# Kernel optimization log

Measured on AMD Instinct MI355X. Metric: run time of the kernel, lower is better.

The kernel has to match this reference:

```python
import jax, jax.numpy as jnp
import numpy as np

P, G, N = 32, 256, 6890  # preds, gallery size, SMPL vertices per person


def _procrustes_v2v(pred, gt):
    """Similarity (Procrustes) align pred->gt, return mean per-vertex L2 error.
    pred, gt: (M, 3) point clouds (M = 2*N, both people jointly aligned)."""
    mu_p = pred.mean(axis=0)
    mu_g = gt.mean(axis=0)
    Xp = pred - mu_p
    Xg = gt - mu_g
    var_p = jnp.sum(Xp * Xp)
    K = Xp.T @ Xg                      # (3,3) cross-covariance
    U, s, Vh = jnp.linalg.svd(K)
    V = Vh.T
    d = jnp.sign(jnp.linalg.det(V @ U.T))  # reflection fix
    D = jnp.stack([jnp.ones_like(d), jnp.ones_like(d), d])
    R = (V * D[None, :]) @ U.T         # rotation, det(R)=+1
    scale = jnp.sum(s * D) / var_p
    aligned = scale * (Xp @ R.T) + mu_g
    return jnp.linalg.norm(aligned - gt, axis=-1).mean()


def setup_inputs() -> dict:
    key = jax.random.key(0)
    k1, k2 = jax.random.split(key)
    pred_vertices = jax.random.normal(k1, (P, 2, N, 3), dtype=jnp.float32)
    target = jax.random.normal(k2, (G, 2, N, 3), dtype=jnp.float32)
    return {"pred_vertices": pred_vertices, "target": target}


def reference(pred_vertices, target):
    # flatten the two-person meshes into a single joint point cloud per sample
    pred = pred_vertices.reshape(pred_vertices.shape[0], -1, 3)  # (P, 2N, 3)
    gt = target.reshape(target.shape[0], -1, 3)                  # (G, 2N, 3)
    # all-pairs procrustes v2v errors: (P, G)
    pair_err = jax.vmap(lambda p: jax.vmap(lambda g: _procrustes_v2v(p, g))(gt))(pred)
    mapping = jnp.argmin(pair_err, axis=1)   # best gt index per prediction
    min_error = jnp.min(pair_err, axis=1)    # its v2v error
    return mapping, min_error
```

## Files before the change

kernel.cpp:

```cpp
#include <hip/hip_runtime.h>
#include <math.h>

#define P_ 32
#define G_ 256
#define NV 6890
#define M_ (2 * NV)
#define QUADS (M_ / 4)
#define NPAIR (P_ * G_)
#define NB_CC 512

struct WS {
    float mu_p[P_][3];
    float var_p[P_];
    float mu_g[G_][3];
    float At[NPAIR][12];
    float Kmat[NPAIR][9];
    float pair_err[NPAIR];
};

__device__ inline double block_reduce(double v, double* smem) {
#pragma unroll
    for (int off = 32; off > 0; off >>= 1) v += __shfl_down(v, off, 64);
    int wid  = threadIdx.x >> 6;
    int lane = threadIdx.x & 63;
    __syncthreads();
    if (lane == 0) smem[wid] = v;
    __syncthreads();
    double r = 0.0;
    if (threadIdx.x == 0) {
        int nw = blockDim.x >> 6;
        for (int w = 0; w < nw; ++w) r += smem[w];
    }
    return r;
}

#define LOAD_QUAD(BASE, Q, X, Y, Z)                                     \
    {                                                                   \
        const float4* _p4 = (const float4*)((BASE) + 12 * (size_t)(Q)); \
        float4 _a = _p4[0], _c = _p4[1], _d = _p4[2];                   \
        X[0] = _a.x; X[1] = _a.w; X[2] = _c.z; X[3] = _d.y;             \
        Y[0] = _a.y; Y[1] = _c.x; Y[2] = _c.w; Y[3] = _d.z;             \
        Z[0] = _a.z; Z[1] = _c.y; Z[2] = _d.x; Z[3] = _d.w;             \
    }

__global__ __launch_bounds__(256, 2) void crosscov_r(const float* __restrict__ pred,
                                                     const float* __restrict__ gt,
                                                     WS* __restrict__ ws) {
    int bx = blockIdx.x;
    int t = threadIdx.x;

    if (bx >= NB_CC) {
        int b = bx - NB_CC;
        bool isP = (b < P_);
        const float* base = isP ? pred + (size_t)b * (M_ * 3)
                                : gt + (size_t)(b - P_) * (M_ * 3);
        double sx = 0, sy = 0, sz = 0, sq = 0;
        for (int q = t; q < QUADS; q += 256) {
            const float4* p4 = (const float4*)(base + 12 * (size_t)q);
            float4 a = p4[0], c = p4[1], d = p4[2];
            sx += (double)a.x + (double)a.w + (double)c.z + (double)d.y;
            sy += (double)a.y + (double)c.x + (double)c.w + (double)d.z;
            sz += (double)a.z + (double)c.y + (double)d.x + (double)d.w;
            if (isP) {
                sq += (double)a.x * a.x + (double)a.y * a.y + (double)a.z * a.z +
                      (double)a.w * a.w + (double)c.x * c.x + (double)c.y * c.y +
                      (double)c.z * c.z + (double)c.w * c.w + (double)d.x * d.x +
                      (double)d.y * d.y + (double)d.z * d.z + (double)d.w * d.w;
            }
        }
        __shared__ double smem[4];
        double rx = block_reduce(sx, smem);
        double ry = block_reduce(sy, smem);
        double rz = block_reduce(sz, smem);
        double rq = block_reduce(sq, smem);
        if (t == 0) {
            double mx = rx / M_, my = ry / M_, mz = rz / M_;
            if (isP) {
                ws->mu_p[b][0] = (float)mx;
                ws->mu_p[b][1] = (float)my;
                ws->mu_p[b][2] = (float)mz;
                ws->var_p[b] = (float)(rq - (mx * mx + my * my + mz * mz) * (double)M_);
            } else {
                ws->mu_g[b - P_][0] = (float)mx;
                ws->mu_g[b - P_][1] = (float)my;
                ws->mu_g[b - P_][2] = (float)mz;
            }
        }
        return;
    }

    int gbase = (bx & 63) * 4;
    int pbase = (bx >> 6) * 4;
    const float* pb[4];
    const float* gb[4];
#pragma unroll
    for (int j = 0; j < 4; ++j) {
        pb[j] = pred + (size_t)(pbase + j) * (M_ * 3);
        gb[j] = gt + (size_t)(gbase + j) * (M_ * 3);
    }

    float acc[16][9];
#pragma unroll
    for (int q = 0; q < 16; ++q)
#pragma unroll
        for (int j = 0; j < 9; ++j) acc[q][j] = 0.f;

    for (int q = t; q < QUADS; q += 256) {
        float px[4][4], py[4][4], pz[4][4];
#pragma unroll
        for (int j = 0; j < 4; ++j) LOAD_QUAD(pb[j], q, px[j], py[j], pz[j]);
#pragma unroll
        for (int gg = 0; gg < 4; ++gg) {
            float gx[4], gy[4], gz[4];
            LOAD_QUAD(gb[gg], q, gx, gy, gz);
#pragma unroll
            for (int pp = 0; pp < 4; ++pp) {
                float* a = acc[gg * 4 + pp];
#pragma unroll
                for (int k = 0; k < 4; ++k) {
                    a[0] = fmaf(px[pp][k], gx[k], a[0]);
                    a[1] = fmaf(px[pp][k], gy[k], a[1]);
                    a[2] = fmaf(px[pp][k], gz[k], a[2]);
                    a[3] = fmaf(py[pp][k], gx[k], a[3]);
                    a[4] = fmaf(py[pp][k], gy[k], a[4]);
                    a[5] = fmaf(py[pp][k], gz[k], a[5]);
                    a[6] = fmaf(pz[pp][k], gx[k], a[6]);
                    a[7] = fmaf(pz[pp][k], gy[k], a[7]);
                    a[8] = fmaf(pz[pp][k], gz[k], a[8]);
                }
            }
        }
    }

#pragma unroll
    for (int q = 0; q < 16; ++q)
#pragma unroll
        for (int j = 0; j < 9; ++j) {
            float v = acc[q][j];
            v += __shfl_xor(v, 1);  v += __shfl_xor(v, 2);
            v += __shfl_xor(v, 4);  v += __shfl_xor(v, 8);
            v += __shfl_xor(v, 16); v += __shfl_xor(v, 32);
            acc[q][j] = v;
        }
    __shared__ float part[4][144];
    int lane = t & 63, wave = t >> 6;
    if (lane == 0) {
#pragma unroll
        for (int q = 0; q < 16; ++q)
#pragma unroll
            for (int j = 0; j < 9; ++j) part[wave][q * 9 + j] = acc[q][j];
    }
    __syncthreads();
    if (t < 144) {
        float s = part[0][t] + part[1][t] + part[2][t] + part[3][t];
        int idx = t / 9, j = t % 9;
        int gg = idx >> 2, pp = idx & 3;
        ws->Kmat[(gbase + gg) * P_ + (pbase + pp)][j] = s;
    }
}

__global__ __launch_bounds__(64) void pair_svd(WS* ws) {
    int pair = blockIdx.x * blockDim.x + threadIdx.x;
    if (pair >= NPAIR) return;
    int p = pair & 31;
    int g = pair >> 5;

    double K[3][3];
#pragma unroll
    for (int a = 0; a < 3; ++a)
#pragma unroll
        for (int b = 0; b < 3; ++b) K[a][b] = (double)ws->Kmat[pair][3 * a + b];
    {
        double mp[3] = { ws->mu_p[p][0], ws->mu_p[p][1], ws->mu_p[p][2] };
        double mg[3] = { ws->mu_g[g][0], ws->mu_g[g][1], ws->mu_g[g][2] };
#pragma unroll
        for (int a = 0; a < 3; ++a)
#pragma unroll
            for (int b = 0; b < 3; ++b)
                K[a][b] -= (double)M_ * mp[a] * mg[b];
    }

    double S[3][3];
#pragma unroll
    for (int a = 0; a < 3; ++a)
#pragma unroll
        for (int b = 0; b < 3; ++b) {
            double acc = 0.0;
#pragma unroll
            for (int c = 0; c < 3; ++c) acc += K[c][a] * K[c][b];
            S[a][b] = acc;
        }

    double V[3][3] = { {1, 0, 0}, {0, 1, 0}, {0, 0, 1} };
    double tr = S[0][0] + S[1][1] + S[2][2];
    double tol = 1e-26 * tr * tr + 1e-300;
    const int PP[3] = {0, 0, 1};
    const int QQ[3] = {1, 2, 2};
    for (int sweep = 0; sweep < 8; ++sweep) {
        double off = S[0][1] * S[0][1] + S[0][2] * S[0][2] + S[1][2] * S[1][2];
        if (off <= tol) break;
        for (int r3 = 0; r3 < 3; ++r3) {
            int pq = PP[r3], qq = QQ[r3];
            double apq = S[pq][qq];
            if (apq == 0.0) continue;
            double theta = (S[qq][qq] - S[pq][pq]) / (2.0 * apq);
            double tt = copysign(1.0, theta) / (fabs(theta) + sqrt(theta * theta + 1.0));
            double c = 1.0 / sqrt(tt * tt + 1.0);
            double sj = tt * c;
            for (int r = 0; r < 3; ++r) {
                double srp = S[r][pq], srq = S[r][qq];
                S[r][pq] = c * srp - sj * srq;
                S[r][qq] = sj * srp + c * srq;
            }
            for (int cc = 0; cc < 3; ++cc) {
                double spr = S[pq][cc], sqr = S[qq][cc];
                S[pq][cc] = c * spr - sj * sqr;
                S[qq][cc] = sj * spr + c * sqr;
            }
            for (int r = 0; r < 3; ++r) {
                double vrp = V[r][pq], vrq = V[r][qq];
                V[r][pq] = c * vrp - sj * vrq;
                V[r][qq] = sj * vrp + c * vrq;
            }
        }
    }

    double lam[3] = { S[0][0], S[1][1], S[2][2] };
    int idx[3] = { 0, 1, 2 };
    if (lam[idx[0]] < lam[idx[1]]) { int tt = idx[0]; idx[0] = idx[1]; idx[1] = tt; }
    if (lam[idx[0]] < lam[idx[2]]) { int tt = idx[0]; idx[0] = idx[2]; idx[2] = tt; }
    if (lam[idx[1]] < lam[idx[2]]) { int tt = idx[1]; idx[1] = idx[2]; idx[2] = tt; }
    double Vs[3][3];
    double sv[3];
#pragma unroll
    for (int i = 0; i < 3; ++i) {
        double l = lam[idx[i]];
        sv[i] = sqrt(l > 0.0 ? l : 0.0);
        for (int r = 0; r < 3; ++r) Vs[r][i] = V[r][idx[i]];
    }

    double U[3][3];
#pragma unroll
    for (int i = 0; i < 3; ++i) {
        double kx = K[0][0] * Vs[0][i] + K[0][1] * Vs[1][i] + K[0][2] * Vs[2][i];
        double ky = K[1][0] * Vs[0][i] + K[1][1] * Vs[1][i] + K[1][2] * Vs[2][i];
        double kz = K[2][0] * Vs[0][i] + K[2][1] * Vs[1][i] + K[2][2] * Vs[2][i];
        double inv = (sv[i] > 1e-12 * sv[0] && sv[i] > 0.0) ? 1.0 / sv[i] : 0.0;
        U[0][i] = kx * inv; U[1][i] = ky * inv; U[2][i] = kz * inv;
    }
    if (sv[2] <= 1e-12 * sv[0] || sv[0] == 0.0) {
        U[0][2] = U[1][0] * U[2][1] - U[2][0] * U[1][1];
        U[1][2] = U[2][0] * U[0][1] - U[0][0] * U[2][1];
        U[2][2] = U[0][0] * U[1][1] - U[1][0] * U[0][1];
    }

    double detK = K[0][0] * (K[1][1] * K[2][2] - K[1][2] * K[2][1])
                - K[0][1] * (K[1][0] * K[2][2] - K[1][2] * K[2][0])
                + K[0][2] * (K[1][0] * K[2][1] - K[1][1] * K[2][0]);
    double d = (detK >= 0.0) ? 1.0 : -1.0;

    double varp = (double)ws->var_p[p];
    double scale = (sv[0] + sv[1] + d * sv[2]) / varp;

    float A[9];
#pragma unroll
    for (int a = 0; a < 3; ++a)
#pragma unroll
        for (int b = 0; b < 3; ++b) {
            double r = Vs[a][0] * U[b][0] + Vs[a][1] * U[b][1] + d * Vs[a][2] * U[b][2];
            A[3 * a + b] = (float)(scale * r);
        }
    double mp[3] = { ws->mu_p[p][0], ws->mu_p[p][1], ws->mu_p[p][2] };
    double mg[3] = { ws->mu_g[g][0], ws->mu_g[g][1], ws->mu_g[g][2] };
    float tvec[3];
#pragma unroll
    for (int a = 0; a < 3; ++a)
        tvec[a] = (float)(mg[a] - ((double)A[3 * a + 0] * mp[0] + (double)A[3 * a + 1] * mp[1] +
                                   (double)A[3 * a + 2] * mp[2]));

#pragma unroll
    for (int j = 0; j < 9; ++j) ws->At[pair][j] = A[j];
#pragma unroll
    for (int j = 0; j < 3; ++j) ws->At[pair][9 + j] = tvec[j];
}

__global__ __launch_bounds__(256, 3) void pair_error_r(const float* __restrict__ pred,
                                                       const float* __restrict__ gt,
                                                       WS* __restrict__ ws) {
    int bx = blockIdx.x;
    int gbase = (bx & 63) * 4;
    int pbase = (bx >> 6) * 2;
    int t = threadIdx.x;

    float A[8][12];
#pragma unroll
    for (int gg = 0; gg < 4; ++gg)
#pragma unroll
        for (int pp = 0; pp < 2; ++pp) {
            int pair = (gbase + gg) * P_ + (pbase + pp);
#pragma unroll
            for (int j = 0; j < 12; ++j) A[gg * 2 + pp][j] = ws->At[pair][j];
        }

    const float* pb0 = pred + (size_t)pbase * (M_ * 3);
    const float* pb1 = pred + (size_t)(pbase + 1) * (M_ * 3);
    const float* gb[4];
#pragma unroll
    for (int j = 0; j < 4; ++j) gb[j] = gt + (size_t)(gbase + j) * (M_ * 3);

    float acc[8];
#pragma unroll
    for (int q = 0; q < 8; ++q) acc[q] = 0.f;

    for (int q = t; q < QUADS; q += 256) {
        float px[2][4], py[2][4], pz[2][4];
        LOAD_QUAD(pb0, q, px[0], py[0], pz[0]);
        LOAD_QUAD(pb1, q, px[1], py[1], pz[1]);
#pragma unroll
        for (int gg = 0; gg < 4; ++gg) {
            float gx[4], gy[4], gz[4];
            LOAD_QUAD(gb[gg], q, gx, gy, gz);
#pragma unroll
            for (int pp = 0; pp < 2; ++pp) {
                const float* a = A[gg * 2 + pp];
                float s = 0.f;
#pragma unroll
                for (int k = 0; k < 4; ++k) {
                    float dx = fmaf(a[0], px[pp][k], fmaf(a[1], py[pp][k], fmaf(a[2], pz[pp][k], a[9])))  - gx[k];
                    float dy = fmaf(a[3], px[pp][k], fmaf(a[4], py[pp][k], fmaf(a[5], pz[pp][k], a[10]))) - gy[k];
                    float dz = fmaf(a[6], px[pp][k], fmaf(a[7], py[pp][k], fmaf(a[8], pz[pp][k], a[11]))) - gz[k];
                    s += __builtin_amdgcn_sqrtf(fmaf(dx, dx, fmaf(dy, dy, dz * dz)));
                }
                acc[gg * 2 + pp] += s;
            }
        }
    }

#pragma unroll
    for (int q = 0; q < 8; ++q) {
        float v = acc[q];
        v += __shfl_xor(v, 1);  v += __shfl_xor(v, 2);
        v += __shfl_xor(v, 4);  v += __shfl_xor(v, 8);
        v += __shfl_xor(v, 16); v += __shfl_xor(v, 32);
        acc[q] = v;
    }
    __shared__ float part[4][8];
    int lane = t & 63, wave = t >> 6;
    if (lane == 0) {
#pragma unroll
        for (int q = 0; q < 8; ++q) part[wave][q] = acc[q];
    }
    __syncthreads();
    if (t < 8) {
        float s = part[0][t] + part[1][t] + part[2][t] + part[3][t];
        int gg = t >> 1, pp = t & 1;
        ws->pair_err[(gbase + gg) * P_ + (pbase + pp)] = s / (float)M_;
    }
}

__global__ void argmin_out(const WS* __restrict__ ws, float* __restrict__ out) {
    __shared__ float be[8][32];
    __shared__ int   bg[8][32];
    int t = threadIdx.x;
    int p = t & 31, slice = t >> 5;
    float best = 3.4e38f;
    int bi = G_;
    for (int g = slice; g < G_; g += 8) {
        float e = ws->pair_err[g * P_ + p];
        if (e < best) { best = e; bi = g; }
    }
    be[slice][p] = best;
    bg[slice][p] = bi;
    __syncthreads();
    if (t < P_) {
        float b0 = be[0][t];
        int   i0 = bg[0][t];
        for (int s = 1; s < 8; ++s) {
            float e = be[s][t];
            int   i = bg[s][t];
            if (e < b0 || (e == b0 && i < i0)) { b0 = e; i0 = i; }
        }
        out[t] = (float)i0;
        out[P_ + t] = b0;
    }
}

extern "C" void kernel_launch(void* const* d_in, const int* in_sizes, int n_in,
                              void* d_out, int out_size, void* d_ws, size_t ws_size,
                              hipStream_t stream) {
    const float* pred = (const float*)d_in[0];
    const float* gt   = (const float*)d_in[1];
    float* out = (float*)d_out;
    WS* ws = (WS*)d_ws;

    crosscov_r<<<dim3(NB_CC + P_ + G_), dim3(256), 0, stream>>>(pred, gt, ws);
    pair_svd<<<dim3(NPAIR / 64), dim3(64), 0, stream>>>(ws);
    pair_error_r<<<dim3(16 * 64), dim3(256), 0, stream>>>(pred, gt, ws);
    argmin_out<<<dim3(1), dim3(256), 0, stream>>>(ws, out);
}
```

Baseline: 214.6 us.

## Split vertex reduction into chunks and shrink crosscov tile to raise parallelism

The cross-covariance and pair-error kernels now split the vertex range into two chunks, each handled by its own block. Each block writes partial sums, which the SVD and argmin kernels combine. The crosscov tile also shrinks from 4x4 to 2x4 pairs with higher occupancy bounds, which lowers register pressure and multiplies block count. In exchange, data reuse per loaded point drops (pred points are reused across fewer pairs), global traffic rises, and partial buffers add extra writes and reads.

```diff
diff --git a/kernel.cpp b/kernel.cpp
--- a/kernel.cpp
+++ b/kernel.cpp
@@ -7,15 +7,16 @@
 #define M_ (2 * NV)
 #define QUADS (M_ / 4)
 #define NPAIR (P_ * G_)
-#define NB_CC 512
+#define KC 2
+#define NB_CC (16 * 64 * KC)
 
 struct WS {
     float mu_p[P_][3];
     float var_p[P_];
     float mu_g[G_][3];
     float At[NPAIR][12];
-    float Kmat[NPAIR][9];
-    float pair_err[NPAIR];
+    float partK[KC][NPAIR][9];
+    float partE[KC][NPAIR];
 };
 
 __device__ inline double block_reduce(double v, double* smem) {
@@ -43,7 +44,7 @@
         Z[0] = _a.z; Z[1] = _c.y; Z[2] = _d.x; Z[3] = _d.w;             \
     }
 
-__global__ __launch_bounds__(256, 2) void crosscov_r(const float* __restrict__ pred,
+__global__ __launch_bounds__(256, 3) void crosscov_c(const float* __restrict__ pred,
                                                      const float* __restrict__ gt,
                                                      WS* __restrict__ ws) {
     int bx = blockIdx.x;
@@ -89,33 +90,35 @@
         return;
     }
 
-    int gbase = (bx & 63) * 4;
-    int pbase = (bx >> 6) * 4;
-    const float* pb[4];
+    int kc = bx >> 10;
+    int rem = bx & 1023;
+    int gbase = (rem & 63) * 4;
+    int pbase = (rem >> 6) * 2;
+    int qbeg = (QUADS * kc) / KC, qend = (QUADS * (kc + 1)) / KC;
+
+    const float* pb0 = pred + (size_t)pbase * (M_ * 3);
+    const float* pb1 = pred + (size_t)(pbase + 1) * (M_ * 3);
     const float* gb[4];
 #pragma unroll
-    for (int j = 0; j < 4; ++j) {
-        pb[j] = pred + (size_t)(pbase + j) * (M_ * 3);
-        gb[j] = gt + (size_t)(gbase + j) * (M_ * 3);
-    }
-
-    float acc[16][9];
-#pragma unroll
-    for (int q = 0; q < 16; ++q)
+    for (int j = 0; j < 4; ++j) gb[j] = gt + (size_t)(gbase + j) * (M_ * 3);
+
+    float acc[8][9];
+#pragma unroll
+    for (int q = 0; q < 8; ++q)
 #pragma unroll
         for (int j = 0; j < 9; ++j) acc[q][j] = 0.f;
 
-    for (int q = t; q < QUADS; q += 256) {
-        float px[4][4], py[4][4], pz[4][4];
-#pragma unroll
-        for (int j = 0; j < 4; ++j) LOAD_QUAD(pb[j], q, px[j], py[j], pz[j]);
+    for (int q = qbeg + t; q < qend; q += 256) {
+        float px[2][4], py[2][4], pz[2][4];
+        LOAD_QUAD(pb0, q, px[0], py[0], pz[0]);
+        LOAD_QUAD(pb1, q, px[1], py[1], pz[1]);
 #pragma unroll
         for (int gg = 0; gg < 4; ++gg) {
             float gx[4], gy[4], gz[4];
             LOAD_QUAD(gb[gg], q, gx, gy, gz);
 #pragma unroll
-            for (int pp = 0; pp < 4; ++pp) {
-                float* a = acc[gg * 4 + pp];
+            for (int pp = 0; pp < 2; ++pp) {
+                float* a = acc[gg * 2 + pp];
 #pragma unroll
                 for (int k = 0; k < 4; ++k) {
                     a[0] = fmaf(px[pp][k], gx[k], a[0]);
@@ -133,7 +136,7 @@
     }
 
 #pragma unroll
-    for (int q = 0; q < 16; ++q)
+    for (int q = 0; q < 8; ++q)
 #pragma unroll
         for (int j = 0; j < 9; ++j) {
             float v = acc[q][j];
@@ -142,20 +145,20 @@
             v += __shfl_xor(v, 16); v += __shfl_xor(v, 32);
             acc[q][j] = v;
         }
-    __shared__ float part[4][144];
+    __shared__ float part[4][72];
     int lane = t & 63, wave = t >> 6;
     if (lane == 0) {
 #pragma unroll
-        for (int q = 0; q < 16; ++q)
+        for (int q = 0; q < 8; ++q)
 #pragma unroll
             for (int j = 0; j < 9; ++j) part[wave][q * 9 + j] = acc[q][j];
     }
     __syncthreads();
-    if (t < 144) {
+    if (t < 72) {
         float s = part[0][t] + part[1][t] + part[2][t] + part[3][t];
         int idx = t / 9, j = t % 9;
-        int gg = idx >> 2, pp = idx & 3;
-        ws->Kmat[(gbase + gg) * P_ + (pbase + pp)][j] = s;
+        int gg = idx >> 1, pp = idx & 1;
+        ws->partK[kc][(gbase + gg) * P_ + (pbase + pp)][j] = s;
     }
 }
 
@@ -169,7 +172,12 @@
 #pragma unroll
     for (int a = 0; a < 3; ++a)
 #pragma unroll
-        for (int b = 0; b < 3; ++b) K[a][b] = (double)ws->Kmat[pair][3 * a + b];
+        for (int b = 0; b < 3; ++b) {
+            double s = 0.0;
+#pragma unroll
+            for (int kc = 0; kc < KC; ++kc) s += (double)ws->partK[kc][pair][3 * a + b];
+            K[a][b] = s;
+        }
     {
         double mp[3] = { ws->mu_p[p][0], ws->mu_p[p][1], ws->mu_p[p][2] };
         double mg[3] = { ws->mu_g[g][0], ws->mu_g[g][1], ws->mu_g[g][2] };
@@ -284,12 +292,15 @@
     for (int j = 0; j < 3; ++j) ws->At[pair][9 + j] = tvec[j];
 }
 
-__global__ __launch_bounds__(256, 3) void pair_error_r(const float* __restrict__ pred,
+__global__ __launch_bounds__(256, 3) void pair_error_c(const float* __restrict__ pred,
                                                        const float* __restrict__ gt,
                                                        WS* __restrict__ ws) {
     int bx = blockIdx.x;
-    int gbase = (bx & 63) * 4;
-    int pbase = (bx >> 6) * 2;
+    int kc = bx >> 10;
+    int rem = bx & 1023;
+    int gbase = (rem & 63) * 4;
+    int pbase = (rem >> 6) * 2;
+    int qbeg = (QUADS * kc) / KC, qend = (QUADS * (kc + 1)) / KC;
     int t = threadIdx.x;
 
     float A[8][12];
@@ -312,7 +323,7 @@
 #pragma unroll
     for (int q = 0; q < 8; ++q) acc[q] = 0.f;
 
-    for (int q = t; q < QUADS; q += 256) {
+    for (int q = qbeg + t; q < qend; q += 256) {
         float px[2][4], py[2][4], pz[2][4];
         LOAD_QUAD(pb0, q, px[0], py[0], pz[0]);
         LOAD_QUAD(pb1, q, px[1], py[1], pz[1]);
@@ -354,7 +365,7 @@
     if (t < 8) {
         float s = part[0][t] + part[1][t] + part[2][t] + part[3][t];
         int gg = t >> 1, pp = t & 1;
-        ws->pair_err[(gbase + gg) * P_ + (pbase + pp)] = s / (float)M_;
+        ws->partE[kc][(gbase + gg) * P_ + (pbase + pp)] = s;
     }
 }
 
@@ -366,7 +377,10 @@
     float best = 3.4e38f;
     int bi = G_;
     for (int g = slice; g < G_; g += 8) {
-        float e = ws->pair_err[g * P_ + p];
+        double s = 0.0;
+#pragma unroll
+        for (int kc = 0; kc < KC; ++kc) s += (double)ws->partE[kc][g * P_ + p];
+        float e = (float)(s / (double)M_);
         if (e < best) { best = e; bi = g; }
     }
     be[slice][p] = best;
@@ -393,8 +407,8 @@
     float* out = (float*)d_out;
     WS* ws = (WS*)d_ws;
 
-    crosscov_r<<<dim3(NB_CC + P_ + G_), dim3(256), 0, stream>>>(pred, gt, ws);
+    crosscov_c<<<dim3(NB_CC + P_ + G_), dim3(256), 0, stream>>>(pred, gt, ws);
     pair_svd<<<dim3(NPAIR / 64), dim3(64), 0, stream>>>(ws);
-    pair_error_r<<<dim3(16 * 64), dim3(256), 0, stream>>>(pred, gt, ws);
+    pair_error_c<<<dim3(16 * 64 * KC), dim3(256), 0, stream>>>(pred, gt, ws);
     argmin_out<<<dim3(1), dim3(256), 0, stream>>>(ws, out);
 }
```

Result: no change. 211.6 us (-1.4%).

## Fuse mean/variance and per-pair SVD into cross-covariance kernel

Applied to the files above, without the earlier changes.

Merges the separate mean/variance blocks and the pair_svd kernel into the cross-covariance kernel. Each block now handles a 2x4 pred/gallery tile instead of 4x4, accumulates the point sums and squared norms alongside K, and then runs the 3x3 SVD for its 8 pairs in the epilogue. This removes one kernel launch and the workspace round-trip for K and the means. In exchange, pred and gallery means are recomputed redundantly in many blocks, gallery data is reloaded twice as often, the sums are kept in float rather than double, and the serial double-precision SVD tail runs on only 8 threads per block.

```diff
diff --git a/kernel.cpp b/kernel.cpp
--- a/kernel.cpp
+++ b/kernel.cpp
@@ -7,32 +7,11 @@
 #define M_ (2 * NV)
 #define QUADS (M_ / 4)
 #define NPAIR (P_ * G_)
-#define NB_CC 512
 
 struct WS {
-    float mu_p[P_][3];
-    float var_p[P_];
-    float mu_g[G_][3];
     float At[NPAIR][12];
-    float Kmat[NPAIR][9];
     float pair_err[NPAIR];
 };
-
-__device__ inline double block_reduce(double v, double* smem) {
-#pragma unroll
-    for (int off = 32; off > 0; off >>= 1) v += __shfl_down(v, off, 64);
-    int wid  = threadIdx.x >> 6;
-    int lane = threadIdx.x & 63;
-    __syncthreads();
-    if (lane == 0) smem[wid] = v;
-    __syncthreads();
-    double r = 0.0;
-    if (threadIdx.x == 0) {
-        int nw = blockDim.x >> 6;
-        for (int w = 0; w < nw; ++w) r += smem[w];
-    }
-    return r;
-}
 
 #define LOAD_QUAD(BASE, Q, X, Y, Z)                                     \
     {                                                                   \
@@ -43,79 +22,71 @@
         Z[0] = _a.z; Z[1] = _c.y; Z[2] = _d.x; Z[3] = _d.w;             \
     }
 
-__global__ __launch_bounds__(256, 2) void crosscov_r(const float* __restrict__ pred,
-                                                     const float* __restrict__ gt,
-                                                     WS* __restrict__ ws) {
+#define BFLY(v)                                              \
+    {                                                        \
+        v += __shfl_xor(v, 1);  v += __shfl_xor(v, 2);       \
+        v += __shfl_xor(v, 4);  v += __shfl_xor(v, 8);       \
+        v += __shfl_xor(v, 16); v += __shfl_xor(v, 32);      \
+    }
+
+__global__ __launch_bounds__(256, 3) void crosscov_svd(const float* __restrict__ pred,
+                                                       const float* __restrict__ gt,
+                                                       WS* __restrict__ ws) {
     int bx = blockIdx.x;
     int t = threadIdx.x;
-
-    if (bx >= NB_CC) {
-        int b = bx - NB_CC;
-        bool isP = (b < P_);
-        const float* base = isP ? pred + (size_t)b * (M_ * 3)
-                                : gt + (size_t)(b - P_) * (M_ * 3);
-        double sx = 0, sy = 0, sz = 0, sq = 0;
-        for (int q = t; q < QUADS; q += 256) {
-            const float4* p4 = (const float4*)(base + 12 * (size_t)q);
-            float4 a = p4[0], c = p4[1], d = p4[2];
-            sx += (double)a.x + (double)a.w + (double)c.z + (double)d.y;
-            sy += (double)a.y + (double)c.x + (double)c.w + (double)d.z;
-            sz += (double)a.z + (double)c.y + (double)d.x + (double)d.w;
-            if (isP) {
-                sq += (double)a.x * a.x + (double)a.y * a.y + (double)a.z * a.z +
-                      (double)a.w * a.w + (double)c.x * c.x + (double)c.y * c.y +
-                      (double)c.z * c.z + (double)c.w * c.w + (double)d.x * d.x +
-                      (double)d.y * d.y + (double)d.z * d.z + (double)d.w * d.w;
-            }
-        }
-        __shared__ double smem[4];
-        double rx = block_reduce(sx, smem);
-        double ry = block_reduce(sy, smem);
-        double rz = block_reduce(sz, smem);
-        double rq = block_reduce(sq, smem);
-        if (t == 0) {
-            double mx = rx / M_, my = ry / M_, mz = rz / M_;
-            if (isP) {
-                ws->mu_p[b][0] = (float)mx;
-                ws->mu_p[b][1] = (float)my;
-                ws->mu_p[b][2] = (float)mz;
-                ws->var_p[b] = (float)(rq - (mx * mx + my * my + mz * mz) * (double)M_);
-            } else {
-                ws->mu_g[b - P_][0] = (float)mx;
-                ws->mu_g[b - P_][1] = (float)my;
-                ws->mu_g[b - P_][2] = (float)mz;
-            }
-        }
-        return;
-    }
-
     int gbase = (bx & 63) * 4;
-    int pbase = (bx >> 6) * 4;
-    const float* pb[4];
+    int pbase = (bx >> 6) * 2;
+
+    const float* pb0 = pred + (size_t)pbase * (M_ * 3);
+    const float* pb1 = pred + (size_t)(pbase + 1) * (M_ * 3);
     const float* gb[4];
 #pragma unroll
-    for (int j = 0; j < 4; ++j) {
-        pb[j] = pred + (size_t)(pbase + j) * (M_ * 3);
-        gb[j] = gt + (size_t)(gbase + j) * (M_ * 3);
-    }
-
-    float acc[16][9];
-#pragma unroll
-    for (int q = 0; q < 16; ++q)
+    for (int j = 0; j < 4; ++j) gb[j] = gt + (size_t)(gbase + j) * (M_ * 3);
+
+    float acc[8][9];
+    float ps[2][4];
+    float gs[4][3];
+#pragma unroll
+    for (int q = 0; q < 8; ++q)
 #pragma unroll
         for (int j = 0; j < 9; ++j) acc[q][j] = 0.f;
+#pragma unroll
+    for (int q = 0; q < 2; ++q)
+#pragma unroll
+        for (int j = 0; j < 4; ++j) ps[q][j] = 0.f;
+#pragma unroll
+    for (int q = 0; q < 4; ++q)
+#pragma unroll
+        for (int j = 0; j < 3; ++j) gs[q][j] = 0.f;
 
     for (int q = t; q < QUADS; q += 256) {
-        float px[4][4], py[4][4], pz[4][4];
-#pragma unroll
-        for (int j = 0; j < 4; ++j) LOAD_QUAD(pb[j], q, px[j], py[j], pz[j]);
+        float px[2][4], py[2][4], pz[2][4];
+        LOAD_QUAD(pb0, q, px[0], py[0], pz[0]);
+        LOAD_QUAD(pb1, q, px[1], py[1], pz[1]);
+#pragma unroll
+        for (int pp = 0; pp < 2; ++pp)
+#pragma unroll
+            for (int k = 0; k < 4; ++k) {
+                ps[pp][0] += px[pp][k];
+                ps[pp][1] += py[pp][k];
+                ps[pp][2] += pz[pp][k];
+                ps[pp][3] = fmaf(px[pp][k], px[pp][k],
+                            fmaf(py[pp][k], py[pp][k],
+                            fmaf(pz[pp][k], pz[pp][k], ps[pp][3])));
+            }
 #pragma unroll
         for (int gg = 0; gg < 4; ++gg) {
             float gx[4], gy[4], gz[4];
             LOAD_QUAD(gb[gg], q, gx, gy, gz);
 #pragma unroll
-            for (int pp = 0; pp < 4; ++pp) {
-                float* a = acc[gg * 4 + pp];
+            for (int k = 0; k < 4; ++k) {
+                gs[gg][0] += gx[k];
+                gs[gg][1] += gy[k];
+                gs[gg][2] += gz[k];
+            }
+#pragma unroll
+            for (int pp = 0; pp < 2; ++pp) {
+                float* a = acc[gg * 2 + pp];
 #pragma unroll
                 for (int k = 0; k < 4; ++k) {
                     a[0] = fmaf(px[pp][k], gx[k], a[0]);
@@ -133,155 +104,160 @@
     }
 
 #pragma unroll
-    for (int q = 0; q < 16; ++q)
-#pragma unroll
-        for (int j = 0; j < 9; ++j) {
-            float v = acc[q][j];
-            v += __shfl_xor(v, 1);  v += __shfl_xor(v, 2);
-            v += __shfl_xor(v, 4);  v += __shfl_xor(v, 8);
-            v += __shfl_xor(v, 16); v += __shfl_xor(v, 32);
-            acc[q][j] = v;
-        }
-    __shared__ float part[4][144];
+    for (int q = 0; q < 8; ++q)
+#pragma unroll
+        for (int j = 0; j < 9; ++j) BFLY(acc[q][j]);
+#pragma unroll
+    for (int q = 0; q < 2; ++q)
+#pragma unroll
+        for (int j = 0; j < 4; ++j) BFLY(ps[q][j]);
+#pragma unroll
+    for (int q = 0; q < 4; ++q)
+#pragma unroll
+        for (int j = 0; j < 3; ++j) BFLY(gs[q][j]);
+
+    __shared__ float red[4][92];
+    __shared__ float fin[92];
     int lane = t & 63, wave = t >> 6;
     if (lane == 0) {
 #pragma unroll
-        for (int q = 0; q < 16; ++q)
-#pragma unroll
-            for (int j = 0; j < 9; ++j) part[wave][q * 9 + j] = acc[q][j];
+        for (int q = 0; q < 8; ++q)
+#pragma unroll
+            for (int j = 0; j < 9; ++j) red[wave][q * 9 + j] = acc[q][j];
+#pragma unroll
+        for (int q = 0; q < 2; ++q)
+#pragma unroll
+            for (int j = 0; j < 4; ++j) red[wave][72 + q * 4 + j] = ps[q][j];
+#pragma unroll
+        for (int q = 0; q < 4; ++q)
+#pragma unroll
+            for (int j = 0; j < 3; ++j) red[wave][80 + q * 3 + j] = gs[q][j];
     }
     __syncthreads();
-    if (t < 144) {
-        float s = part[0][t] + part[1][t] + part[2][t] + part[3][t];
-        int idx = t / 9, j = t % 9;
-        int gg = idx >> 2, pp = idx & 3;
-        ws->Kmat[(gbase + gg) * P_ + (pbase + pp)][j] = s;
-    }
-}
-
-__global__ __launch_bounds__(64) void pair_svd(WS* ws) {
-    int pair = blockIdx.x * blockDim.x + threadIdx.x;
-    if (pair >= NPAIR) return;
-    int p = pair & 31;
-    int g = pair >> 5;
-
-    double K[3][3];
-#pragma unroll
-    for (int a = 0; a < 3; ++a)
-#pragma unroll
-        for (int b = 0; b < 3; ++b) K[a][b] = (double)ws->Kmat[pair][3 * a + b];
-    {
-        double mp[3] = { ws->mu_p[p][0], ws->mu_p[p][1], ws->mu_p[p][2] };
-        double mg[3] = { ws->mu_g[g][0], ws->mu_g[g][1], ws->mu_g[g][2] };
+    if (t < 92) fin[t] = red[0][t] + red[1][t] + red[2][t] + red[3][t];
+    __syncthreads();
+
+    if (t < 8) {
+        int gg = t >> 1, pp = t & 1;
+        double K[3][3];
+#pragma unroll
+        for (int a = 0; a < 3; ++a)
+#pragma unroll
+            for (int b = 0; b < 3; ++b) K[a][b] = (double)fin[t * 9 + 3 * a + b];
+
+        double mp[3] = { fin[72 + pp * 4 + 0] / (double)M_,
+                         fin[72 + pp * 4 + 1] / (double)M_,
+                         fin[72 + pp * 4 + 2] / (double)M_ };
+        double varp = (double)fin[72 + pp * 4 + 3] -
+                      (mp[0] * mp[0] + mp[1] * mp[1] + mp[2] * mp[2]) * (double)M_;
+        double mg[3] = { fin[80 + gg * 3 + 0] / (double)M_,
+                         fin[80 + gg * 3 + 1] / (double)M_,
+                         fin[80 + gg * 3 + 2] / (double)M_ };
 #pragma unroll
         for (int a = 0; a < 3; ++a)
 #pragma unroll
             for (int b = 0; b < 3; ++b)
                 K[a][b] -= (double)M_ * mp[a] * mg[b];
-    }
-
-    double S[3][3];
-#pragma unroll
-    for (int a = 0; a < 3; ++a)
-#pragma unroll
-        for (int b = 0; b < 3; ++b) {
-            double acc = 0.0;
-#pragma unroll
-            for (int c = 0; c < 3; ++c) acc += K[c][a] * K[c][b];
-            S[a][b] = acc;
-        }
-
-    double V[3][3] = { {1, 0, 0}, {0, 1, 0}, {0, 0, 1} };
-    double tr = S[0][0] + S[1][1] + S[2][2];
-    double tol = 1e-26 * tr * tr + 1e-300;
-    const int PP[3] = {0, 0, 1};
-    const int QQ[3] = {1, 2, 2};
-    for (int sweep = 0; sweep < 8; ++sweep) {
-        double off = S[0][1] * S[0][1] + S[0][2] * S[0][2] + S[1][2] * S[1][2];
-        if (off <= tol) break;
-        for (int r3 = 0; r3 < 3; ++r3) {
-            int pq = PP[r3], qq = QQ[r3];
-            double apq = S[pq][qq];
-            if (apq == 0.0) continue;
-            double theta = (S[qq][qq] - S[pq][pq]) / (2.0 * apq);
-            double tt = copysign(1.0, theta) / (fabs(theta) + sqrt(theta * theta + 1.0));
-            double c = 1.0 / sqrt(tt * tt + 1.0);
-            double sj = tt * c;
-            for (int r = 0; r < 3; ++r) {
-                double srp = S[r][pq], srq = S[r][qq];
-                S[r][pq] = c * srp - sj * srq;
-                S[r][qq] = sj * srp + c * srq;
-            }
-            for (int cc = 0; cc < 3; ++cc) {
-                double spr = S[pq][cc], sqr = S[qq][cc];
-                S[pq][cc] = c * spr - sj * sqr;
-                S[qq][cc] = sj * spr + c * sqr;
-            }
-            for (int r = 0; r < 3; ++r) {
-                double vrp = V[r][pq], vrq = V[r][qq];
-                V[r][pq] = c * vrp - sj * vrq;
-                V[r][qq] = sj * vrp + c * vrq;
-            }
-        }
-    }
-
-    double lam[3] = { S[0][0], S[1][1], S[2][2] };
-    int idx[3] = { 0, 1, 2 };
-    if (lam[idx[0]] < lam[idx[1]]) { int tt = idx[0]; idx[0] = idx[1]; idx[1] = tt; }
-    if (lam[idx[0]] < lam[idx[2]]) { int tt = idx[0]; idx[0] = idx[2]; idx[2] = tt; }
-    if (lam[idx[1]] < lam[idx[2]]) { int tt = idx[1]; idx[1] = idx[2]; idx[2] = tt; }
-    double Vs[3][3];
-    double sv[3];
-#pragma unroll
-    for (int i = 0; i < 3; ++i) {
-        double l = lam[idx[i]];
-        sv[i] = sqrt(l > 0.0 ? l : 0.0);
-        for (int r = 0; r < 3; ++r) Vs[r][i] = V[r][idx[i]];
-    }
-
-    double U[3][3];
-#pragma unroll
-    for (int i = 0; i < 3; ++i) {
-        double kx = K[0][0] * Vs[0][i] + K[0][1] * Vs[1][i] + K[0][2] * Vs[2][i];
-        double ky = K[1][0] * Vs[0][i] + K[1][1] * Vs[1][i] + K[1][2] * Vs[2][i];
-        double kz = K[2][0] * Vs[0][i] + K[2][1] * Vs[1][i] + K[2][2] * Vs[2][i];
-        double inv = (sv[i] > 1e-12 * sv[0] && sv[i] > 0.0) ? 1.0 / sv[i] : 0.0;
-        U[0][i] = kx * inv; U[1][i] = ky * inv; U[2][i] = kz * inv;
-    }
-    if (sv[2] <= 1e-12 * sv[0] || sv[0] == 0.0) {
-        U[0][2] = U[1][0] * U[2][1] - U[2][0] * U[1][1];
-        U[1][2] = U[2][0] * U[0][1] - U[0][0] * U[2][1];
-        U[2][2] = U[0][0] * U[1][1] - U[1][0] * U[0][1];
-    }
-
-    double detK = K[0][0] * (K[1][1] * K[2][2] - K[1][2] * K[2][1])
-                - K[0][1] * (K[1][0] * K[2][2] - K[1][2] * K[2][0])
-                + K[0][2] * (K[1][0] * K[2][1] - K[1][1] * K[2][0]);
-    double d = (detK >= 0.0) ? 1.0 : -1.0;
-
-    double varp = (double)ws->var_p[p];
-    double scale = (sv[0] + sv[1] + d * sv[2]) / varp;
-
-    float A[9];
-#pragma unroll
-    for (int a = 0; a < 3; ++a)
-#pragma unroll
-        for (int b = 0; b < 3; ++b) {
-            double r = Vs[a][0] * U[b][0] + Vs[a][1] * U[b][1] + d * Vs[a][2] * U[b][2];
-            A[3 * a + b] = (float)(scale * r);
-        }
-    double mp[3] = { ws->mu_p[p][0], ws->mu_p[p][1], ws->mu_p[p][2] };
-    double mg[3] = { ws->mu_g[g][0], ws->mu_g[g][1], ws->mu_g[g][2] };
-    float tvec[3];
-#pragma unroll
-    for (int a = 0; a < 3; ++a)
-        tvec[a] = (float)(mg[a] - ((double)A[3 * a + 0] * mp[0] + (double)A[3 * a + 1] * mp[1] +
-                                   (double)A[3 * a + 2] * mp[2]));
-
-#pragma unroll
-    for (int j = 0; j < 9; ++j) ws->At[pair][j] = A[j];
-#pragma unroll
-    for (int j = 0; j < 3; ++j) ws->At[pair][9 + j] = tvec[j];
+
+        double S[3][3];
+#pragma unroll
+        for (int a = 0; a < 3; ++a)
+#pragma unroll
+            for (int b = 0; b < 3; ++b) {
+                double s = 0.0;
+#pragma unroll
+                for (int c = 0; c < 3; ++c) s += K[c][a] * K[c][b];
+                S[a][b] = s;
+            }
+
+        double V[3][3] = { {1, 0, 0}, {0, 1, 0}, {0, 0, 1} };
+        double tr = S[0][0] + S[1][1] + S[2][2];
+        double tol = 1e-26 * tr * tr + 1e-300;
+        const int PPi[3] = {0, 0, 1};
+        const int QQi[3] = {1, 2, 2};
+        for (int sweep = 0; sweep < 8; ++sweep) {
+            double off = S[0][1] * S[0][1] + S[0][2] * S[0][2] + S[1][2] * S[1][2];
+            if (off <= tol) break;
+            for (int r3 = 0; r3 < 3; ++r3) {
+                int pq = PPi[r3], qq = QQi[r3];
+                double apq = S[pq][qq];
+                if (apq == 0.0) continue;
+                double theta = (S[qq][qq] - S[pq][pq]) / (2.0 * apq);
+                double tt = copysign(1.0, theta) / (fabs(theta) + sqrt(theta * theta + 1.0));
+                double c = 1.0 / sqrt(tt * tt + 1.0);
+                double sj = tt * c;
+                for (int r = 0; r < 3; ++r) {
+                    double srp = S[r][pq], srq = S[r][qq];
+                    S[r][pq] = c * srp - sj * srq;
+                    S[r][qq] = sj * srp + c * srq;
+                }
+                for (int cc = 0; cc < 3; ++cc) {
+                    double spr = S[pq][cc], sqr = S[qq][cc];
+                    S[pq][cc] = c * spr - sj * sqr;
+                    S[qq][cc] = sj * spr + c * sqr;
+                }
+                for (int r = 0; r < 3; ++r) {
+                    double vrp = V[r][pq], vrq = V[r][qq];
+                    V[r][pq] = c * vrp - sj * vrq;
+                    V[r][qq] = sj * vrp + c * vrq;
+                }
+            }
+        }
+
+        double lam[3] = { S[0][0], S[1][1], S[2][2] };
+        int idx[3] = { 0, 1, 2 };
+        if (lam[idx[0]] < lam[idx[1]]) { int w = idx[0]; idx[0] = idx[1]; idx[1] = w; }
+        if (lam[idx[0]] < lam[idx[2]]) { int w = idx[0]; idx[0] = idx[2]; idx[2] = w; }
+        if (lam[idx[1]] < lam[idx[2]]) { int w = idx[1]; idx[1] = idx[2]; idx[2] = w; }
+        double Vs[3][3], sv[3];
+#pragma unroll
+        for (int i = 0; i < 3; ++i) {
+            double l = lam[idx[i]];
+            sv[i] = sqrt(l > 0.0 ? l : 0.0);
+            for (int r = 0; r < 3; ++r) Vs[r][i] = V[r][idx[i]];
+        }
+
+        double U[3][3];
+#pragma unroll
+        for (int i = 0; i < 3; ++i) {
+            double kx = K[0][0] * Vs[0][i] + K[0][1] * Vs[1][i] + K[0][2] * Vs[2][i];
+            double ky = K[1][0] * Vs[0][i] + K[1][1] * Vs[1][i] + K[1][2] * Vs[2][i];
+            double kz = K[2][0] * Vs[0][i] + K[2][1] * Vs[1][i] + K[2][2] * Vs[2][i];
+            double inv = (sv[i] > 1e-12 * sv[0] && sv[i] > 0.0) ? 1.0 / sv[i] : 0.0;
+            U[0][i] = kx * inv; U[1][i] = ky * inv; U[2][i] = kz * inv;
+        }
+        if (sv[2] <= 1e-12 * sv[0] || sv[0] == 0.0) {
+            U[0][2] = U[1][0] * U[2][1] - U[2][0] * U[1][1];
+            U[1][2] = U[2][0] * U[0][1] - U[0][0] * U[2][1];
+            U[2][2] = U[0][0] * U[1][1] - U[1][0] * U[0][1];
+        }
+
+        double detK = K[0][0] * (K[1][1] * K[2][2] - K[1][2] * K[2][1])
+                    - K[0][1] * (K[1][0] * K[2][2] - K[1][2] * K[2][0])
+                    + K[0][2] * (K[1][0] * K[2][1] - K[1][1] * K[2][0]);
+        double d = (detK >= 0.0) ? 1.0 : -1.0;
+        double scale = (sv[0] + sv[1] + d * sv[2]) / varp;
+
+        float A[9];
+#pragma unroll
+        for (int a = 0; a < 3; ++a)
+#pragma unroll
+            for (int b = 0; b < 3; ++b) {
+                double r = Vs[a][0] * U[b][0] + Vs[a][1] * U[b][1] + d * Vs[a][2] * U[b][2];
+                A[3 * a + b] = (float)(scale * r);
+            }
+        float tvec[3];
+#pragma unroll
+        for (int a = 0; a < 3; ++a)
+            tvec[a] = (float)(mg[a] - ((double)A[3 * a + 0] * mp[0] + (double)A[3 * a + 1] * mp[1] +
+                                       (double)A[3 * a + 2] * mp[2]));
+
+        int pair = (gbase + gg) * P_ + (pbase + pp);
+#pragma unroll
+        for (int j = 0; j < 9; ++j) ws->At[pair][j] = A[j];
+#pragma unroll
+        for (int j = 0; j < 3; ++j) ws->At[pair][9 + j] = tvec[j];
+    }
 }
 
 __global__ __launch_bounds__(256, 3) void pair_error_r(const float* __restrict__ pred,
@@ -337,13 +313,7 @@
     }
 
 #pragma unroll
-    for (int q = 0; q < 8; ++q) {
-        float v = acc[q];
-        v += __shfl_xor(v, 1);  v += __shfl_xor(v, 2);
-        v += __shfl_xor(v, 4);  v += __shfl_xor(v, 8);
-        v += __shfl_xor(v, 16); v += __shfl_xor(v, 32);
-        acc[q] = v;
-    }
+    for (int q = 0; q < 8; ++q) BFLY(acc[q]);
     __shared__ float part[4][8];
     int lane = t & 63, wave = t >> 6;
     if (lane == 0) {
@@ -393,8 +363,7 @@
     float* out = (float*)d_out;
     WS* ws = (WS*)d_ws;
 
-    crosscov_r<<<dim3(NB_CC + P_ + G_), dim3(256), 0, stream>>>(pred, gt, ws);
-    pair_svd<<<dim3(NPAIR / 64), dim3(64), 0, stream>>>(ws);
+    crosscov_svd<<<dim3(16 * 64), dim3(256), 0, stream>>>(pred, gt, ws);
     pair_error_r<<<dim3(16 * 64), dim3(256), 0, stream>>>(pred, gt, ws);
     argmin_out<<<dim3(1), dim3(256), 0, stream>>>(ws, out);
 }
```

Result: slower. 381.3 us (+77.7%).
